# Performance work log

Measured on AMD Instinct MI355X. Metric: run time of the kernel, lower is better.

Reference implementation:

```python
import jax, jax.numpy as jnp
import numpy as np

EMB = 1024

def setup_inputs() -> dict:
    key = jax.random.key(0)
    ks = jax.random.split(key, 6)
    T, k1, k2, D = 64, 256, 1024, EMB
    scale = 1.0 / np.sqrt(D)
    return {
        "fast_feature": jax.random.normal(ks[0], (T, k2, D), jnp.float32),
        "slow_feature": jax.random.normal(ks[1], (T, k1, D), jnp.float32),
        "fast_W": jax.random.normal(ks[2], (D, D), jnp.float32) * scale,
        "fast_b": jax.random.normal(ks[3], (D,), jnp.float32) * 0.01,
        "slow_W": jax.random.normal(ks[4], (D, D), jnp.float32) * scale,
        "slow_b": jax.random.normal(ks[5], (D,), jnp.float32) * 0.01,
    }

def reference(fast_feature, slow_feature, fast_W, fast_b, slow_W, slow_b):
    # Linear projections (torch Linear: x @ W.T + b)
    fast_key = jnp.einsum('tkd,ed->tke', fast_feature, fast_W) + fast_b  # [T,k2,D]
    slow_key = jnp.einsum('tkd,ed->tke', slow_feature, slow_W) + slow_b  # [T,k1,D]
    # Scaled dot-product similarity fast->slow
    sim = jnp.einsum('tqd,tkd->tqk', fast_key, slow_key)  # [T,k2,k1]
    sim = sim / jnp.sqrt(jnp.asarray(slow_feature.shape[-1], sim.dtype))
    attn = jax.nn.softmax(sim, axis=-1)
    ctx = jnp.einsum('tqk,tkd->tqd', attn, slow_feature)  # note: values are raw slow_feature
    return fast_feature + ctx
```

## Files before the change

kernel.cpp:

```cpp
#include <hip/hip_runtime.h>
#include <stdint.h>

typedef __attribute__((ext_vector_type(8))) short bf16x8;
typedef __attribute__((ext_vector_type(4))) float f32x4;

__device__ __forceinline__ unsigned short f2bf(float f) {
  unsigned int u = __builtin_bit_cast(unsigned int, f);
  u += 0x7FFFu + ((u >> 16) & 1u);
  return (unsigned short)(u >> 16);
}

__device__ __forceinline__ void gload_lds16(const void* g, void* l) {
  __builtin_amdgcn_global_load_lds(
      (__attribute__((address_space(1))) void*)(uintptr_t)g,
      (__attribute__((address_space(3))) void*)l,
      16, 0, 0);
}

#define BARRIER() do { asm volatile("" ::: "memory"); __builtin_amdgcn_s_barrier(); asm volatile("" ::: "memory"); } while (0)
#define WAITVM(N) asm volatile("s_waitcnt vmcnt(" #N ")" ::: "memory")

template <int MODE>
__global__ __launch_bounds__(512, 2) void gemm8(
    const unsigned short* __restrict__ A, const unsigned short* __restrict__ B,
    void* __restrict__ Cv, const float* __restrict__ aux, int N, int K,
    int nm, int nn, long sAB, long sBB, long sCB, long sXB, float scale)
{
  __shared__ __align__(16) char lds[131072];
  char* ldsc = lds;

  const int tid = threadIdx.x;
  const int lane = tid & 63;
  const int wid = tid >> 6;
  const int fr = lane & 15, fq = lane >> 4;

  const int nwg = gridDim.x;
  const int id = blockIdx.x;
  const int swz = (id & 7) * (nwg >> 3) + (id >> 3);
  const int per = nm * nn;
  const int t = swz / per;
  const int rem = swz - t * per;
  const int mi_ = rem / nn, ni_ = rem - mi_ * nn;
  const long bm = (long)mi_ * 256, bn = (long)ni_ * 256;

  const unsigned short* Ag = A + (long)t * sAB + bm * K;
  const unsigned short* Bg = B + (long)t * sBB + bn * K;
  const int NT = K >> 6;

  const unsigned short* aS[2][2];
  const unsigned short* bS[2][2];
#pragma unroll
  for (int p = 0; p < 2; ++p) {
    const int q = p * 512 + tid;
    const int lr = q >> 3, cs = q & 7;
    const int cl = cs ^ (lr & 7);
#pragma unroll
    for (int h = 0; h < 2; ++h) {
      const int gA = ((lr >> 6) << 7) | (h << 6) | (lr & 63);
      const int gB = ((lr >> 5) << 6) | (h << 5) | (lr & 31);
      aS[p][h] = Ag + (long)gA * K + cl * 8;
      bS[p][h] = Bg + (long)gB * K + cl * 8;
    }
  }

  const int c0 = ((fq ^ (fr & 3)) + ((fr >> 2) & 1) * 4) * 16;
  const int aRd = ((wid >> 2) * 64 + fr) * 128 + c0;
  const int bRd = ((wid & 3) * 32 + fr) * 128 + c0;

  f32x4 acc[2][2][4][2];
#pragma unroll
  for (int a = 0; a < 2; a++)
#pragma unroll
    for (int b = 0; b < 2; b++)
#pragma unroll
      for (int i = 0; i < 4; i++)
#pragma unroll
        for (int j = 0; j < 2; j++)
#pragma unroll
          for (int r = 0; r < 4; r++) acc[a][b][i][j][r] = 0.f;

  bf16x8 af[4][2], bf[2][2][2];

#define STAGE(srcArr, aoff, h, ktv, b) do {                                   \
  _Pragma("unroll")                                                           \
  for (int p = 0; p < 2; ++p)                                                 \
    gload_lds16(srcArr[p][h] + ((long)(ktv) << 6),                            \
                ldsc + (aoff) + ((b) << 16) + ((h) << 14) + (p << 13) + (wid << 10)); \
} while (0)

#define LDA(mi, cub) do {                                                     \
  _Pragma("unroll")                                                           \
  for (int i = 0; i < 4; ++i) {                                               \
    af[i][0] = *(const bf16x8*)(ldsc + (cub) + (mi) * 16384 + aRd + i * 2048);        \
    af[i][1] = *(const bf16x8*)(ldsc + (cub) + (mi) * 16384 + (aRd ^ 64) + i * 2048); \
  }                                                                           \
} while (0)

#define LDB(nj, cub) do {                                                     \
  _Pragma("unroll")                                                           \
  for (int j = 0; j < 2; ++j) {                                               \
    bf[nj][j][0] = *(const bf16x8*)(ldsc + 32768 + (cub) + (nj) * 16384 + bRd + j * 2048);        \
    bf[nj][j][1] = *(const bf16x8*)(ldsc + 32768 + (cub) + (nj) * 16384 + (bRd ^ 64) + j * 2048); \
  }                                                                           \
} while (0)

#define QUAD(mi, nj) do {                                                     \
  __builtin_amdgcn_s_setprio(1);                                              \
  _Pragma("unroll")                                                           \
  for (int i = 0; i < 4; ++i)                                                 \
  _Pragma("unroll")                                                           \
  for (int j = 0; j < 2; ++j) {                                               \
    acc[mi][nj][i][j] = __builtin_amdgcn_mfma_f32_16x16x32_bf16(              \
        af[i][0], bf[nj][j][0], acc[mi][nj][i][j], 0, 0, 0);                  \
    acc[mi][nj][i][j] = __builtin_amdgcn_mfma_f32_16x16x32_bf16(              \
        af[i][1], bf[nj][j][1], acc[mi][nj][i][j], 0, 0, 0);                  \
  }                                                                           \
  __builtin_amdgcn_s_setprio(0);                                              \
} while (0)

  STAGE(aS, 0, 0, 0, 0);
  STAGE(bS, 32768, 0, 0, 0);
  STAGE(bS, 32768, 1, 0, 0);
  STAGE(aS, 0, 1, 0, 0);
  if (NT > 1) {
    STAGE(aS, 0, 0, 1, 1);
    STAGE(bS, 32768, 0, 1, 1);
    STAGE(bS, 32768, 1, 1, 1);
    WAITVM(6);
  } else {
    WAITVM(0);
  }
  BARRIER();

  for (int kt = 0; kt < NT; ++kt) {
    const int cur = kt & 1, nxt = cur ^ 1;
    const int cub = cur << 16;
    LDA(0, cub);
    LDB(0, cub);
    if (kt + 1 < NT) STAGE(aS, 0, 1, kt + 1, nxt);
    BARRIER();
    QUAD(0, 0);
    BARRIER();
    LDB(1, cub);
    if (kt + 2 < NT) STAGE(aS, 0, 0, kt + 2, cur);
    BARRIER();
    QUAD(0, 1);
    BARRIER();
    LDA(1, cub);
    if (kt + 2 < NT) STAGE(bS, 32768, 0, kt + 2, cur);
    BARRIER();
    QUAD(1, 0);
    BARRIER();
    if (kt + 2 < NT) {
      STAGE(bS, 32768, 1, kt + 2, cur);
      QUAD(1, 1);
      WAITVM(6);
    } else {
      QUAD(1, 1);
      WAITVM(0);
    }
    BARRIER();
  }

#pragma unroll
  for (int mi = 0; mi < 2; ++mi)
#pragma unroll
    for (int nj = 0; nj < 2; ++nj)
#pragma unroll
      for (int i = 0; i < 4; ++i) {
        const long grow0 = bm + (wid >> 2) * 128 + mi * 64 + i * 16 + fq * 4;
#pragma unroll
        for (int j = 0; j < 2; ++j) {
          const long gcol = bn + (wid & 3) * 64 + nj * 32 + j * 16 + fr;
          if (MODE == 0) {
            unsigned short* C = (unsigned short*)Cv + (long)t * sCB;
            const float bv = aux[gcol];
#pragma unroll
            for (int r = 0; r < 4; ++r)
              C[(grow0 + r) * N + gcol] = f2bf(acc[mi][nj][i][j][r] + bv);
          } else if (MODE == 1) {
            float* C = (float*)Cv + (long)t * sCB;
#pragma unroll
            for (int r = 0; r < 4; ++r)
              C[(grow0 + r) * N + gcol] = acc[mi][nj][i][j][r] * scale;
          } else {
            float* C = (float*)Cv + (long)t * sCB;
            const float* X = aux + (long)t * sXB;
#pragma unroll
            for (int r = 0; r < 4; ++r) {
              const long idx = (grow0 + r) * N + gcol;
              C[idx] = acc[mi][nj][i][j][r] + X[idx];
            }
          }
        }
      }
#undef STAGE
#undef LDA
#undef LDB
#undef QUAD
}

__global__ __launch_bounds__(256) void convert_f32_bf16(
    const float* __restrict__ in, unsigned short* __restrict__ out, long n) {
  long i = ((long)blockIdx.x * 256 + threadIdx.x) * 4;
  long stride = (long)gridDim.x * 1024;
  for (; i < n; i += stride) {
    float4 v = *(const float4*)(in + i);
    ushort4 o;
    o.x = f2bf(v.x); o.y = f2bf(v.y); o.z = f2bf(v.z); o.w = f2bf(v.w);
    *(ushort4*)(out + i) = o;
  }
}

__global__ __launch_bounds__(256) void transpose_slow_bf16(
    const float* __restrict__ in, unsigned short* __restrict__ out) {
  __shared__ unsigned short tile[32][33];
  int t = blockIdx.z;
  int d0 = blockIdx.x * 32;
  int k0 = blockIdx.y * 32;
  const float* ip = in + (long)t * 256 * 1024;
  unsigned short* op = out + (long)t * 1024 * 256;
  int tx = threadIdx.x & 31, ty = threadIdx.x >> 5;
#pragma unroll
  for (int p = 0; p < 4; p++) {
    int k = ty + p * 8;
    tile[k][tx] = f2bf(ip[(long)(k0 + k) * 1024 + d0 + tx]);
  }
  __syncthreads();
#pragma unroll
  for (int p = 0; p < 4; p++) {
    int d = ty + p * 8;
    op[(long)(d0 + d) * 256 + k0 + tx] = tile[tx][d];
  }
}

__global__ __launch_bounds__(256) void softmax256(
    const float* __restrict__ sim, unsigned short* __restrict__ attn) {
  int row = blockIdx.x * 4 + (threadIdx.x >> 6);
  int lane = threadIdx.x & 63;
  const float4 v = *(const float4*)(sim + (long)row * 256 + lane * 4);
  float m = fmaxf(fmaxf(v.x, v.y), fmaxf(v.z, v.w));
#pragma unroll
  for (int o = 32; o >= 1; o >>= 1) m = fmaxf(m, __shfl_xor(m, o));
  float e0 = __expf(v.x - m), e1 = __expf(v.y - m);
  float e2 = __expf(v.z - m), e3 = __expf(v.w - m);
  float s = e0 + e1 + e2 + e3;
#pragma unroll
  for (int o = 32; o >= 1; o >>= 1) s += __shfl_xor(s, o);
  float inv = 1.0f / s;
  ushort4 o4;
  o4.x = f2bf(e0 * inv); o4.y = f2bf(e1 * inv);
  o4.z = f2bf(e2 * inv); o4.w = f2bf(e3 * inv);
  *(ushort4*)(attn + (long)row * 256 + lane * 4) = o4;
}

extern "C" void kernel_launch(void* const* d_in, const int* in_sizes, int n_in,
                              void* d_out, int out_size, void* d_ws, size_t ws_size,
                              hipStream_t stream) {
  const float* fastF     = (const float*)d_in[0];
  const float* slowF     = (const float*)d_in[1];
  const float* fastW     = (const float*)d_in[2];
  const float* fast_bias = (const float*)d_in[3];
  const float* slowW     = (const float*)d_in[4];
  const float* slow_bias = (const float*)d_in[5];
  float* out = (float*)d_out;

  char* ws = (char*)d_ws;
  unsigned short* fastBf  = (unsigned short*)(ws);
  float*          sim     = (float*)(ws);
  unsigned short* attnBf  = (unsigned short*)(ws + 67108864L);
  unsigned short* fastKey = (unsigned short*)(ws + 134217728L);
  unsigned short* slowBf  = (unsigned short*)(ws + 268435456L);
  unsigned short* slowT   = (unsigned short*)(ws + 301989888L);
  unsigned short* slowKey = (unsigned short*)(ws + 335544320L);
  unsigned short* fWb     = (unsigned short*)(ws + 369098752L);
  unsigned short* sWb     = (unsigned short*)(ws + 371195904L);

  convert_f32_bf16<<<2048, 256, 0, stream>>>(fastF, fastBf, 67108864L);
  convert_f32_bf16<<<2048, 256, 0, stream>>>(slowF, slowBf, 16777216L);
  convert_f32_bf16<<<1024, 256, 0, stream>>>(fastW, fWb, 1048576L);
  convert_f32_bf16<<<1024, 256, 0, stream>>>(slowW, sWb, 1048576L);
  transpose_slow_bf16<<<dim3(32, 8, 64), 256, 0, stream>>>(slowF, slowT);

  gemm8<0><<<64 * 4, 512, 0, stream>>>(slowBf, sWb, slowKey, slow_bias,
      1024, 1024, 64, 4, 0, 0, 0, 0, 1.f);
  gemm8<0><<<256 * 4, 512, 0, stream>>>(fastBf, fWb, fastKey, fast_bias,
      1024, 1024, 256, 4, 0, 0, 0, 0, 1.f);
  gemm8<1><<<4 * 1 * 64, 512, 0, stream>>>(fastKey, slowKey, sim, nullptr,
      256, 1024, 4, 1, 1048576L, 262144L, 262144L, 0, 0.03125f);
  softmax256<<<16384, 256, 0, stream>>>(sim, attnBf);
  gemm8<2><<<4 * 4 * 64, 512, 0, stream>>>(attnBf, slowT, out, fastF,
      1024, 256, 4, 4, 262144L, 262144L, 1048576L, 1048576L, 1.f);
}
```

Measured before the change: 497.4 us.

## Software-pipeline LDS fragment loads across k-tiles and store sim logits as bf16

```diff
diff --git a/kernel.cpp b/kernel.cpp
--- a/kernel.cpp
+++ b/kernel.cpp
@@ -8,6 +8,10 @@
   unsigned int u = __builtin_bit_cast(unsigned int, f);
   u += 0x7FFFu + ((u >> 16) & 1u);
   return (unsigned short)(u >> 16);
+}
+
+__device__ __forceinline__ float bf2f(unsigned short s) {
+  return __builtin_bit_cast(float, (unsigned int)s << 16);
 }
 
 __device__ __forceinline__ void gload_lds16(const void* g, void* l) {
@@ -79,7 +83,7 @@
 #pragma unroll
           for (int r = 0; r < 4; r++) acc[a][b][i][j][r] = 0.f;
 
-  bf16x8 af[4][2], bf[2][2][2];
+  bf16x8 af[2][4][2], bf[2][2][2];
 
 #define STAGE(srcArr, aoff, h, ktv, b) do {                                   \
   _Pragma("unroll")                                                           \
@@ -88,19 +92,19 @@
                 ldsc + (aoff) + ((b) << 16) + ((h) << 14) + (p << 13) + (wid << 10)); \
 } while (0)
 
-#define LDA(mi, cub) do {                                                     \
+#define LDA(mi, bb) do {                                                      \
   _Pragma("unroll")                                                           \
   for (int i = 0; i < 4; ++i) {                                               \
-    af[i][0] = *(const bf16x8*)(ldsc + (cub) + (mi) * 16384 + aRd + i * 2048);        \
-    af[i][1] = *(const bf16x8*)(ldsc + (cub) + (mi) * 16384 + (aRd ^ 64) + i * 2048); \
+    af[mi][i][0] = *(const bf16x8*)(ldsc + (bb) + (mi) * 16384 + aRd + i * 2048);        \
+    af[mi][i][1] = *(const bf16x8*)(ldsc + (bb) + (mi) * 16384 + (aRd ^ 64) + i * 2048); \
   }                                                                           \
 } while (0)
 
-#define LDB(nj, cub) do {                                                     \
+#define LDB(nj, bb) do {                                                      \
   _Pragma("unroll")                                                           \
   for (int j = 0; j < 2; ++j) {                                               \
-    bf[nj][j][0] = *(const bf16x8*)(ldsc + 32768 + (cub) + (nj) * 16384 + bRd + j * 2048);        \
-    bf[nj][j][1] = *(const bf16x8*)(ldsc + 32768 + (cub) + (nj) * 16384 + (bRd ^ 64) + j * 2048); \
+    bf[nj][j][0] = *(const bf16x8*)(ldsc + 32768 + (bb) + (nj) * 16384 + bRd + j * 2048);        \
+    bf[nj][j][1] = *(const bf16x8*)(ldsc + 32768 + (bb) + (nj) * 16384 + (bRd ^ 64) + j * 2048); \
   }                                                                           \
 } while (0)
 
@@ -111,56 +115,48 @@
   _Pragma("unroll")                                                           \
   for (int j = 0; j < 2; ++j) {                                               \
     acc[mi][nj][i][j] = __builtin_amdgcn_mfma_f32_16x16x32_bf16(              \
-        af[i][0], bf[nj][j][0], acc[mi][nj][i][j], 0, 0, 0);                  \
+        af[mi][i][0], bf[nj][j][0], acc[mi][nj][i][j], 0, 0, 0);              \
     acc[mi][nj][i][j] = __builtin_amdgcn_mfma_f32_16x16x32_bf16(              \
-        af[i][1], bf[nj][j][1], acc[mi][nj][i][j], 0, 0, 0);                  \
+        af[mi][i][1], bf[nj][j][1], acc[mi][nj][i][j], 0, 0, 0);              \
   }                                                                           \
   __builtin_amdgcn_s_setprio(0);                                              \
+} while (0)
+
+#define KT(CUR, TAIL, ktv) do {                                               \
+  if (TAIL == 2) { WAITVM(0); } else { WAITVM(6); }                           \
+  LDB(1, (CUR) << 16);                                                        \
+  if (TAIL != 2) STAGE(aS, 0, 1, (ktv) + 1, (CUR) ^ 1);                       \
+  BARRIER(); QUAD(0, 0); BARRIER();                                           \
+  LDA(1, (CUR) << 16);                                                        \
+  if (TAIL == 0) STAGE(aS, 0, 0, (ktv) + 2, CUR);                             \
+  BARRIER(); QUAD(0, 1); BARRIER();                                           \
+  if (TAIL == 0) { WAITVM(6); } else if (TAIL == 1) { WAITVM(4); }            \
+  if (TAIL == 0) STAGE(bS, 32768, 0, (ktv) + 2, CUR);                         \
+  BARRIER(); QUAD(1, 0); BARRIER();                                           \
+  if (TAIL == 0) { WAITVM(6); } else if (TAIL == 1) { WAITVM(2); }            \
+  if (TAIL != 2) { LDA(0, ((CUR) ^ 1) << 16); LDB(0, ((CUR) ^ 1) << 16); }    \
+  if (TAIL == 0) STAGE(bS, 32768, 1, (ktv) + 2, CUR);                         \
+  BARRIER(); QUAD(1, 1); BARRIER();                                           \
 } while (0)
 
   STAGE(aS, 0, 0, 0, 0);
   STAGE(bS, 32768, 0, 0, 0);
   STAGE(bS, 32768, 1, 0, 0);
   STAGE(aS, 0, 1, 0, 0);
-  if (NT > 1) {
-    STAGE(aS, 0, 0, 1, 1);
-    STAGE(bS, 32768, 0, 1, 1);
-    STAGE(bS, 32768, 1, 1, 1);
-    WAITVM(6);
-  } else {
-    WAITVM(0);
-  }
+  STAGE(aS, 0, 0, 1, 1);
+  STAGE(bS, 32768, 0, 1, 1);
+  STAGE(bS, 32768, 1, 1, 1);
+  WAITVM(8);
   BARRIER();
-
-  for (int kt = 0; kt < NT; ++kt) {
-    const int cur = kt & 1, nxt = cur ^ 1;
-    const int cub = cur << 16;
-    LDA(0, cub);
-    LDB(0, cub);
-    if (kt + 1 < NT) STAGE(aS, 0, 1, kt + 1, nxt);
-    BARRIER();
-    QUAD(0, 0);
-    BARRIER();
-    LDB(1, cub);
-    if (kt + 2 < NT) STAGE(aS, 0, 0, kt + 2, cur);
-    BARRIER();
-    QUAD(0, 1);
-    BARRIER();
-    LDA(1, cub);
-    if (kt + 2 < NT) STAGE(bS, 32768, 0, kt + 2, cur);
-    BARRIER();
-    QUAD(1, 0);
-    BARRIER();
-    if (kt + 2 < NT) {
-      STAGE(bS, 32768, 1, kt + 2, cur);
-      QUAD(1, 1);
-      WAITVM(6);
-    } else {
-      QUAD(1, 1);
-      WAITVM(0);
-    }
-    BARRIER();
-  }
+  LDA(0, 0);
+  LDB(0, 0);
+
+  for (int kt = 0; kt + 2 < NT; kt += 2) {
+    KT(0, 0, kt);
+    KT(1, 0, kt + 1);
+  }
+  KT(0, 1, NT - 2);
+  KT(1, 2, NT - 1);
 
 #pragma unroll
   for (int mi = 0; mi < 2; ++mi)
@@ -179,10 +175,10 @@
             for (int r = 0; r < 4; ++r)
               C[(grow0 + r) * N + gcol] = f2bf(acc[mi][nj][i][j][r] + bv);
           } else if (MODE == 1) {
-            float* C = (float*)Cv + (long)t * sCB;
+            unsigned short* C = (unsigned short*)Cv + (long)t * sCB;
 #pragma unroll
             for (int r = 0; r < 4; ++r)
-              C[(grow0 + r) * N + gcol] = acc[mi][nj][i][j][r] * scale;
+              C[(grow0 + r) * N + gcol] = f2bf(acc[mi][nj][i][j][r] * scale);
           } else {
             float* C = (float*)Cv + (long)t * sCB;
             const float* X = aux + (long)t * sXB;
@@ -198,6 +194,7 @@
 #undef LDA
 #undef LDB
 #undef QUAD
+#undef KT
 }
 
 __global__ __launch_bounds__(256) void convert_f32_bf16(
@@ -235,15 +232,16 @@
 }
 
 __global__ __launch_bounds__(256) void softmax256(
-    const float* __restrict__ sim, unsigned short* __restrict__ attn) {
+    const unsigned short* __restrict__ sim, unsigned short* __restrict__ attn) {
   int row = blockIdx.x * 4 + (threadIdx.x >> 6);
   int lane = threadIdx.x & 63;
-  const float4 v = *(const float4*)(sim + (long)row * 256 + lane * 4);
-  float m = fmaxf(fmaxf(v.x, v.y), fmaxf(v.z, v.w));
+  const ushort4 u = *(const ushort4*)(sim + (long)row * 256 + lane * 4);
+  float v0 = bf2f(u.x), v1 = bf2f(u.y), v2 = bf2f(u.z), v3 = bf2f(u.w);
+  float m = fmaxf(fmaxf(v0, v1), fmaxf(v2, v3));
 #pragma unroll
   for (int o = 32; o >= 1; o >>= 1) m = fmaxf(m, __shfl_xor(m, o));
-  float e0 = __expf(v.x - m), e1 = __expf(v.y - m);
-  float e2 = __expf(v.z - m), e3 = __expf(v.w - m);
+  float e0 = __expf(v0 - m), e1 = __expf(v1 - m);
+  float e2 = __expf(v2 - m), e3 = __expf(v3 - m);
   float s = e0 + e1 + e2 + e3;
 #pragma unroll
   for (int o = 32; o >= 1; o >>= 1) s += __shfl_xor(s, o);
@@ -267,7 +265,7 @@
 
   char* ws = (char*)d_ws;
   unsigned short* fastBf  = (unsigned short*)(ws);
-  float*          sim     = (float*)(ws);
+  unsigned short* simB    = (unsigned short*)(ws);
   unsigned short* attnBf  = (unsigned short*)(ws + 67108864L);
   unsigned short* fastKey = (unsigned short*)(ws + 134217728L);
   unsigned short* slowBf  = (unsigned short*)(ws + 268435456L);
@@ -286,9 +284,9 @@
       1024, 1024, 64, 4, 0, 0, 0, 0, 1.f);
   gemm8<0><<<256 * 4, 512, 0, stream>>>(fastBf, fWb, fastKey, fast_bias,
       1024, 1024, 256, 4, 0, 0, 0, 0, 1.f);
-  gemm8<1><<<4 * 1 * 64, 512, 0, stream>>>(fastKey, slowKey, sim, nullptr,
+  gemm8<1><<<4 * 1 * 64, 512, 0, stream>>>(fastKey, slowKey, simB, nullptr,
       256, 1024, 4, 1, 1048576L, 262144L, 262144L, 0, 0.03125f);
-  softmax256<<<16384, 256, 0, stream>>>(sim, attnBf);
+  softmax256<<<16384, 256, 0, stream>>>(simB, attnBf);
   gemm8<2><<<4 * 4 * 64, 512, 0, stream>>>(attnBf, slowT, out, fastF,
       1024, 256, 4, 4, 262144L, 262144L, 1048576L, 1048576L, 1.f);
 }
```

New measurement: 712.8 us. 1.43x slower.

## Fuse softmax into similarity GEMM epilogue and merge slow convert with transpose

Applied to the files above, without the earlier changes.

```diff
diff --git a/kernel.cpp b/kernel.cpp
--- a/kernel.cpp
+++ b/kernel.cpp
@@ -162,38 +162,95 @@
     BARRIER();
   }
 
-#pragma unroll
-  for (int mi = 0; mi < 2; ++mi)
-#pragma unroll
-    for (int nj = 0; nj < 2; ++nj)
-#pragma unroll
-      for (int i = 0; i < 4; ++i) {
-        const long grow0 = bm + (wid >> 2) * 128 + mi * 64 + i * 16 + fq * 4;
-#pragma unroll
-        for (int j = 0; j < 2; ++j) {
-          const long gcol = bn + (wid & 3) * 64 + nj * 32 + j * 16 + fr;
-          if (MODE == 0) {
-            unsigned short* C = (unsigned short*)Cv + (long)t * sCB;
-            const float bv = aux[gcol];
-#pragma unroll
-            for (int r = 0; r < 4; ++r)
-              C[(grow0 + r) * N + gcol] = f2bf(acc[mi][nj][i][j][r] + bv);
-          } else if (MODE == 1) {
-            float* C = (float*)Cv + (long)t * sCB;
-#pragma unroll
-            for (int r = 0; r < 4; ++r)
-              C[(grow0 + r) * N + gcol] = acc[mi][nj][i][j][r] * scale;
-          } else {
-            float* C = (float*)Cv + (long)t * sCB;
-            const float* X = aux + (long)t * sXB;
-#pragma unroll
-            for (int r = 0; r < 4; ++r) {
-              const long idx = (grow0 + r) * N + gcol;
-              C[idx] = acc[mi][nj][i][j][r] + X[idx];
+  if (MODE == 1) {
+    float* red  = (float*)ldsc;
+    float* red2 = (float*)(ldsc + 4096);
+    const int wc = wid & 3;
+    const int rbase = (wid >> 2) * 128;
+#pragma unroll
+    for (int mi = 0; mi < 2; ++mi)
+#pragma unroll
+      for (int i = 0; i < 4; ++i)
+#pragma unroll
+        for (int r = 0; r < 4; ++r) {
+          float m = fmaxf(fmaxf(acc[mi][0][i][0][r], acc[mi][0][i][1][r]),
+                          fmaxf(acc[mi][1][i][0][r], acc[mi][1][i][1][r]));
+#pragma unroll
+          for (int o = 1; o <= 8; o <<= 1) m = fmaxf(m, __shfl_xor(m, o));
+          if (fr == 0) red[(rbase + mi * 64 + i * 16 + fq * 4 + r) * 4 + wc] = m;
+        }
+    BARRIER();
+#pragma unroll
+    for (int mi = 0; mi < 2; ++mi)
+#pragma unroll
+      for (int i = 0; i < 4; ++i)
+#pragma unroll
+        for (int r = 0; r < 4; ++r) {
+          const int rl = rbase + mi * 64 + i * 16 + fq * 4 + r;
+          f32x4 mm = *(f32x4*)&red[rl * 4];
+          const float M = fmaxf(fmaxf(mm[0], mm[1]), fmaxf(mm[2], mm[3]));
+          float s = 0.f;
+#pragma unroll
+          for (int nj = 0; nj < 2; ++nj)
+#pragma unroll
+            for (int j = 0; j < 2; ++j) {
+              float e = __expf((acc[mi][nj][i][j][r] - M) * scale);
+              acc[mi][nj][i][j][r] = e;
+              s += e;
+            }
+#pragma unroll
+          for (int o = 1; o <= 8; o <<= 1) s += __shfl_xor(s, o);
+          if (fr == 0) red2[rl * 4 + wc] = s;
+        }
+    BARRIER();
+    unsigned short* C = (unsigned short*)Cv + (long)t * sCB;
+#pragma unroll
+    for (int mi = 0; mi < 2; ++mi)
+#pragma unroll
+      for (int i = 0; i < 4; ++i)
+#pragma unroll
+        for (int r = 0; r < 4; ++r) {
+          const int rl = rbase + mi * 64 + i * 16 + fq * 4 + r;
+          f32x4 sv = *(f32x4*)&red2[rl * 4];
+          const float inv = 1.0f / (sv[0] + sv[1] + sv[2] + sv[3]);
+          const long gr = bm + rl;
+#pragma unroll
+          for (int nj = 0; nj < 2; ++nj)
+#pragma unroll
+            for (int j = 0; j < 2; ++j) {
+              const long gcol = bn + wc * 64 + nj * 32 + j * 16 + fr;
+              C[gr * N + gcol] = f2bf(acc[mi][nj][i][j][r] * inv);
+            }
+        }
+  } else {
+#pragma unroll
+    for (int mi = 0; mi < 2; ++mi)
+#pragma unroll
+      for (int nj = 0; nj < 2; ++nj)
+#pragma unroll
+        for (int i = 0; i < 4; ++i) {
+          const long grow0 = bm + (wid >> 2) * 128 + mi * 64 + i * 16 + fq * 4;
+#pragma unroll
+          for (int j = 0; j < 2; ++j) {
+            const long gcol = bn + (wid & 3) * 64 + nj * 32 + j * 16 + fr;
+            if (MODE == 0) {
+              unsigned short* C = (unsigned short*)Cv + (long)t * sCB;
+              const float bv = aux[gcol];
+#pragma unroll
+              for (int r = 0; r < 4; ++r)
+                C[(grow0 + r) * N + gcol] = f2bf(acc[mi][nj][i][j][r] + bv);
+            } else {
+              float* C = (float*)Cv + (long)t * sCB;
+              const float* X = aux + (long)t * sXB;
+#pragma unroll
+              for (int r = 0; r < 4; ++r) {
+                const long idx = (grow0 + r) * N + gcol;
+                C[idx] = acc[mi][nj][i][j][r] + X[idx];
+              }
             }
           }
         }
-      }
+  }
 #undef STAGE
 #undef LDA
 #undef LDB
@@ -212,46 +269,30 @@
   }
 }
 
-__global__ __launch_bounds__(256) void transpose_slow_bf16(
-    const float* __restrict__ in, unsigned short* __restrict__ out) {
+__global__ __launch_bounds__(256) void convert_transpose_slow(
+    const float* __restrict__ in, unsigned short* __restrict__ outR,
+    unsigned short* __restrict__ outT) {
   __shared__ unsigned short tile[32][33];
   int t = blockIdx.z;
   int d0 = blockIdx.x * 32;
   int k0 = blockIdx.y * 32;
   const float* ip = in + (long)t * 256 * 1024;
-  unsigned short* op = out + (long)t * 1024 * 256;
+  unsigned short* rp = outR + (long)t * 256 * 1024;
+  unsigned short* tp = outT + (long)t * 1024 * 256;
   int tx = threadIdx.x & 31, ty = threadIdx.x >> 5;
 #pragma unroll
   for (int p = 0; p < 4; p++) {
     int k = ty + p * 8;
-    tile[k][tx] = f2bf(ip[(long)(k0 + k) * 1024 + d0 + tx]);
+    unsigned short b = f2bf(ip[(long)(k0 + k) * 1024 + d0 + tx]);
+    tile[k][tx] = b;
+    rp[(long)(k0 + k) * 1024 + d0 + tx] = b;
   }
   __syncthreads();
 #pragma unroll
   for (int p = 0; p < 4; p++) {
     int d = ty + p * 8;
-    op[(long)(d0 + d) * 256 + k0 + tx] = tile[tx][d];
-  }
-}
-
-__global__ __launch_bounds__(256) void softmax256(
-    const float* __restrict__ sim, unsigned short* __restrict__ attn) {
-  int row = blockIdx.x * 4 + (threadIdx.x >> 6);
-  int lane = threadIdx.x & 63;
-  const float4 v = *(const float4*)(sim + (long)row * 256 + lane * 4);
-  float m = fmaxf(fmaxf(v.x, v.y), fmaxf(v.z, v.w));
-#pragma unroll
-  for (int o = 32; o >= 1; o >>= 1) m = fmaxf(m, __shfl_xor(m, o));
-  float e0 = __expf(v.x - m), e1 = __expf(v.y - m);
-  float e2 = __expf(v.z - m), e3 = __expf(v.w - m);
-  float s = e0 + e1 + e2 + e3;
-#pragma unroll
-  for (int o = 32; o >= 1; o >>= 1) s += __shfl_xor(s, o);
-  float inv = 1.0f / s;
-  ushort4 o4;
-  o4.x = f2bf(e0 * inv); o4.y = f2bf(e1 * inv);
-  o4.z = f2bf(e2 * inv); o4.w = f2bf(e3 * inv);
-  *(ushort4*)(attn + (long)row * 256 + lane * 4) = o4;
+    tp[(long)(d0 + d) * 256 + k0 + tx] = tile[tx][d];
+  }
 }
 
 extern "C" void kernel_launch(void* const* d_in, const int* in_sizes, int n_in,
@@ -267,7 +308,6 @@
 
   char* ws = (char*)d_ws;
   unsigned short* fastBf  = (unsigned short*)(ws);
-  float*          sim     = (float*)(ws);
   unsigned short* attnBf  = (unsigned short*)(ws + 67108864L);
   unsigned short* fastKey = (unsigned short*)(ws + 134217728L);
   unsigned short* slowBf  = (unsigned short*)(ws + 268435456L);
@@ -277,18 +317,16 @@
   unsigned short* sWb     = (unsigned short*)(ws + 371195904L);
 
   convert_f32_bf16<<<2048, 256, 0, stream>>>(fastF, fastBf, 67108864L);
-  convert_f32_bf16<<<2048, 256, 0, stream>>>(slowF, slowBf, 16777216L);
   convert_f32_bf16<<<1024, 256, 0, stream>>>(fastW, fWb, 1048576L);
   convert_f32_bf16<<<1024, 256, 0, stream>>>(slowW, sWb, 1048576L);
-  transpose_slow_bf16<<<dim3(32, 8, 64), 256, 0, stream>>>(slowF, slowT);
+  convert_transpose_slow<<<dim3(32, 8, 64), 256, 0, stream>>>(slowF, slowBf, slowT);
 
   gemm8<0><<<64 * 4, 512, 0, stream>>>(slowBf, sWb, slowKey, slow_bias,
       1024, 1024, 64, 4, 0, 0, 0, 0, 1.f);
   gemm8<0><<<256 * 4, 512, 0, stream>>>(fastBf, fWb, fastKey, fast_bias,
       1024, 1024, 256, 4, 0, 0, 0, 0, 1.f);
-  gemm8<1><<<4 * 1 * 64, 512, 0, stream>>>(fastKey, slowKey, sim, nullptr,
+  gemm8<1><<<4 * 1 * 64, 512, 0, stream>>>(fastKey, slowKey, attnBf, nullptr,
       256, 1024, 4, 1, 1048576L, 262144L, 262144L, 0, 0.03125f);
-  softmax256<<<16384, 256, 0, stream>>>(sim, attnBf);
   gemm8<2><<<4 * 4 * 64, 512, 0, stream>>>(attnBf, slowT, out, fastF,
       1024, 256, 4, 4, 262144L, 262144L, 1048576L, 1048576L, 1.f);
 }
```

Measured after the change: 478.7 us. 1.04x faster.
